# Kernel optimization log

Hardware: AMD Instinct MI355X
Metric: run time of the kernel (lower is better)

## Reference

```python
import jax, jax.numpy as jnp
import numpy as np

B, L, D = 4, 8192, 512


def setup_inputs() -> dict:
    key = jax.random.key(0)
    kx, kwg, kwc = jax.random.split(key, 3)
    x = jax.random.normal(kx, (B, L, D), dtype=jnp.float32)
    # Xavier-uniform init for DxD linears
    bound = float(np.sqrt(6.0 / (D + D)))
    Wg = jax.random.uniform(kwg, (D, D), minval=-bound, maxval=bound, dtype=jnp.float32)
    bg = jnp.ones((D,), dtype=jnp.float32)   # gate bias init to 1.0
    Wc = jax.random.uniform(kwc, (D, D), minval=-bound, maxval=bound, dtype=jnp.float32)
    bc = jnp.zeros((D,), dtype=jnp.float32)
    return {"x": x, "Wg": Wg, "bg": bg, "Wc": Wc, "bc": bc}


def _mingru_scan(gates, cands):
    # h_t = (1 - g_t) * h_{t-1} + g_t * c_t, h_0 = 0
    # linear recurrence h_t = a_t h_{t-1} + b_t with a = 1-g, b = g*c
    a = 1.0 - gates
    b = gates * cands

    def combine(left, right):
        a_l, b_l = left
        a_r, b_r = right
        return a_r * a_l, a_r * b_l + b_r

    _, h = jax.lax.associative_scan(combine, (a, b), axis=1)
    return h


def reference(x, Wg, bg, Wc, bc):
    gates = jax.nn.sigmoid(jnp.einsum('bld,ed->ble', x, Wg) + bg)
    cands = jnp.tanh(jnp.einsum('bld,ed->ble', x, Wc) + bc)
    return _mingru_scan(gates, cands)
```

## Files before the change

kernel.cpp:

```cpp
#include <hip/hip_runtime.h>
#include <stdint.h>
#include <stddef.h>

#define B_ 4
#define L_ 8192
#define D_ 512
#define M_ (B_*L_)
#define K_ 512
#define CHUNK 64
#define NC (L_/CHUNK)

typedef _Float16 f16;
typedef f16 f16x2 __attribute__((ext_vector_type(2)));
typedef f16 f16x4 __attribute__((ext_vector_type(4)));
typedef f16 f16x8 __attribute__((ext_vector_type(8)));
typedef __fp16 h16x2 __attribute__((ext_vector_type(2)));
typedef float f32x4 __attribute__((ext_vector_type(4)));

__device__ __forceinline__ uint32_t pack2(float a, float b) {
  h16x2 p = __builtin_amdgcn_cvt_pkrtz(a, b);
  return __builtin_bit_cast(uint32_t, p);
}

__device__ __forceinline__ void async16(const void* g, void* l) {
  __builtin_amdgcn_global_load_lds(
      (const __attribute__((address_space(1))) uint32_t*)g,
      (__attribute__((address_space(3))) uint32_t*)l,
      16, 0, 0);
}

__global__ __launch_bounds__(256) void cvt_x(const float* __restrict__ x,
                                             f16* __restrict__ xh) {
  int idx = (blockIdx.x * 256 + threadIdx.x) * 4;
  float4 v = *(const float4*)(x + idx);
  f16x4 o = {(f16)v.x, (f16)v.y, (f16)v.z, (f16)v.w};
  *(f16x4*)(xh + idx) = o;
}

__global__ __launch_bounds__(256) void pack_w(const float* __restrict__ Wg,
                                              const float* __restrict__ Wc,
                                              f16* __restrict__ wp) {
  int idx = (blockIdx.x * 256 + threadIdx.x) * 4;
  const float* src = (idx < 262144) ? (Wg + idx) : (Wc + (idx - 262144));
  float4 v = *(const float4*)src;
  f16x4 o = {(f16)v.x, (f16)v.y, (f16)v.z, (f16)v.w};
  *(f16x4*)(wp + idx) = o;
}

__global__ __launch_bounds__(256, 2) void gemm_act(
    const f16* __restrict__ Xh, const f16* __restrict__ Wp,
    const float* __restrict__ bg, const float* __restrict__ bc,
    uint32_t* __restrict__ AC) {
  __shared__ __align__(16) f16 sA[128 * 32];
  __shared__ __align__(16) f16 sBg[128 * 32];
  __shared__ __align__(16) f16 sBc[128 * 32];

  const int tid = threadIdx.x;
  const int id = blockIdx.x;
  const int xcd = id & 7;
  const int slot = id >> 3;
  const int g_ = xcd * 128 + slot;
  const int bm = g_ >> 2;
  const int bn = g_ & 3;

  const int lane = tid & 63;
  const int w = tid >> 6;
  const int wm = w >> 1, wn = w & 1;
  const int l15 = lane & 15, quad = lane >> 4;

  const int srow = tid >> 2;
  const int spc8 = (tid & 3) * 8;
  const f16* gA  = Xh + (size_t)(bm * 128 + srow) * K_ + spc8;
  const f16* gBg = Wp + (size_t)(bn * 128 + srow) * K_ + spc8;
  const f16* gBc = Wp + (size_t)(512 + bn * 128 + srow) * K_ + spc8;
  f16* lA  = sA  + tid * 8;
  f16* lBg = sBg + tid * 8;
  f16* lBc = sBc + tid * 8;

  f32x4 accG[4][4] = {};
  f32x4 accC[4][4] = {};

  for (int k0 = 0; k0 < K_; k0 += 32) {
    async16(gA + k0,  lA);
    async16(gA + (size_t)64 * K_ + k0,  lA  + 64 * 32);
    async16(gBg + k0, lBg);
    async16(gBg + (size_t)64 * K_ + k0, lBg + 64 * 32);
    async16(gBc + k0, lBc);
    async16(gBc + (size_t)64 * K_ + k0, lBc + 64 * 32);
    __syncthreads();

    f16x8 af[4], bgf[4], bcf[4];
#pragma unroll
    for (int i = 0; i < 4; i++)
      af[i]  = *(const f16x8*)(sA  + (wm * 64 + i * 16 + l15) * 32 + quad * 8);
#pragma unroll
    for (int j = 0; j < 4; j++) {
      bgf[j] = *(const f16x8*)(sBg + (wn * 64 + j * 16 + l15) * 32 + quad * 8);
      bcf[j] = *(const f16x8*)(sBc + (wn * 64 + j * 16 + l15) * 32 + quad * 8);
    }
#pragma unroll
    for (int i = 0; i < 4; i++)
#pragma unroll
      for (int j = 0; j < 4; j++) {
        accG[i][j] = __builtin_amdgcn_mfma_f32_16x16x32_f16(af[i], bgf[j], accG[i][j], 0, 0, 0);
        accC[i][j] = __builtin_amdgcn_mfma_f32_16x16x32_f16(af[i], bcf[j], accC[i][j], 0, 0, 0);
      }
    __syncthreads();
  }

#pragma unroll
  for (int j = 0; j < 4; j++) {
    const int col = bn * 128 + wn * 64 + j * 16 + l15;
    const float bgv = bg[col];
    const float bcv = bc[col];
#pragma unroll
    for (int i = 0; i < 4; i++) {
      const int mrow = bm * 128 + wm * 64 + i * 16 + quad * 4;
#pragma unroll
      for (int r = 0; r < 4; r++) {
        float yg = accG[i][j][r] + bgv;
        float yc = accC[i][j][r] + bcv;
        AC[(size_t)(mrow + r) * 512 + col] = pack2(yg, yc);
      }
    }
  }
}

__global__ __launch_bounds__(512) void scan_local(
    uint32_t* __restrict__ AC,
    float* __restrict__ cA, float* __restrict__ cB) {
  const int blk = blockIdx.x;
  const int d = threadIdx.x;
  const size_t base = (size_t)blk * CHUNK * 512 + d;
  float P = 1.0f, Q = 0.0f;
#pragma unroll 4
  for (int t = 0; t < CHUNK; t++) {
    const size_t i = base + (size_t)t * 512;
    f16x2 v = __builtin_bit_cast(f16x2, AC[i]);
    float yg = (float)v[0];
    float yc = (float)v[1];
    float a = 1.0f / (1.0f + __expf(yg));
    float e = __expf(fmaxf(-2.0f * yc, -30.0f));
    float c = (1.0f - e) / (1.0f + e);
    float b = (1.0f - a) * c;
    AC[i] = pack2(a, b);
    Q = fmaf(a, Q, b);
    P *= a;
  }
  cA[blk * 512 + d] = P;
  cB[blk * 512 + d] = Q;
}

__global__ __launch_bounds__(64) void scan_chunks(
    const float* __restrict__ cA, const float* __restrict__ cB,
    float* __restrict__ Hp) {
  const int b = blockIdx.x >> 3;
  const int d = ((blockIdx.x & 7) << 6) + threadIdx.x;
  float h = 0.0f;
#pragma unroll 8
  for (int ch = 0; ch < NC; ch++) {
    const int idx = (b * NC + ch) * 512 + d;
    Hp[idx] = h;
    h = fmaf(cA[idx], h, cB[idx]);
  }
}

__global__ __launch_bounds__(512) void scan_apply(
    const uint32_t* __restrict__ AC, const float* __restrict__ Hp,
    float* __restrict__ out) {
  const int blk = blockIdx.x;
  const int d = threadIdx.x;
  const size_t base = (size_t)blk * CHUNK * 512 + d;
  float h = Hp[blk * 512 + d];
#pragma unroll 4
  for (int t = 0; t < CHUNK; t++) {
    const size_t i = base + (size_t)t * 512;
    f16x2 v = __builtin_bit_cast(f16x2, AC[i]);
    h = fmaf((float)v[0], h, (float)v[1]);
    out[i] = h;
  }
}

extern "C" void kernel_launch(void* const* d_in, const int* in_sizes, int n_in,
                              void* d_out, int out_size, void* d_ws, size_t ws_size,
                              hipStream_t stream) {
  const float* x  = (const float*)d_in[0];
  const float* Wg = (const float*)d_in[1];
  const float* bg = (const float*)d_in[2];
  const float* Wc = (const float*)d_in[3];
  const float* bc = (const float*)d_in[4];
  float* out = (float*)d_out;

  char* ws = (char*)d_ws;
  f16*      xh = (f16*)(ws);
  f16*      wp = (f16*)(ws + 33554432);
  uint32_t* AC = (uint32_t*)(ws + 34603008);
  float*    cA = (float*)(ws + 101711872);
  float*    cB = (float*)(ws + 102760448);
  float*    Hp = (float*)(ws + 103809024);

  cvt_x<<<M_ * D_ / (256 * 4), 256, 0, stream>>>(x, xh);
  pack_w<<<2 * D_ * D_ / (256 * 4), 256, 0, stream>>>(Wg, Wc, wp);
  gemm_act<<<(M_ / 128) * 4, 256, 0, stream>>>(xh, wp, bg, bc, AC);
  scan_local<<<B_ * NC, 512, 0, stream>>>(AC, cA, cB);
  scan_chunks<<<32, 64, 0, stream>>>(cA, cB, Hp);
  scan_apply<<<B_ * NC, 512, 0, stream>>>(AC, Hp, out);
}
```

Measured before the change: 220.9 us.

## Merge prep kernels, parallelize chunk scan with warp shuffles, recompute activations

Merges the x and weight fp16 conversion kernels into one launch. Replaces the serial per-batch chunk-carry scan (32 blocks of 64 threads walking 128 chunks) with a warp-level shuffle scan, one wavefront per (batch, channel). scan_local no longer writes the activated a/b back to AC; scan_apply recomputes the sigmoid/tanh from the raw pre-activations, trading extra transcendental math for fewer global writes. The GEMM launch bound also goes from 2 to 4 blocks per CU, which may force register spilling given its large accumulator arrays.

```diff
diff --git a/kernel.cpp b/kernel.cpp
--- a/kernel.cpp
+++ b/kernel.cpp
@@ -8,7 +8,7 @@
 #define M_ (B_*L_)
 #define K_ 512
 #define CHUNK 64
-#define NC (L_/CHUNK)
+#define NC_SEQ (L_/CHUNK)
 
 typedef _Float16 f16;
 typedef f16 f16x2 __attribute__((ext_vector_type(2)));
@@ -22,6 +22,16 @@
   return __builtin_bit_cast(uint32_t, p);
 }
 
+__device__ __forceinline__ void act_ab(uint32_t raw, float& a, float& b) {
+  f16x2 v = __builtin_bit_cast(f16x2, raw);
+  float yg = (float)v[0];
+  float yc = (float)v[1];
+  a = 1.0f / (1.0f + __expf(yg));
+  float e = __expf(fmaxf(-2.0f * yc, -30.0f));
+  float c = (1.0f - e) / (1.0f + e);
+  b = (1.0f - a) * c;
+}
+
 __device__ __forceinline__ void async16(const void* g, void* l) {
   __builtin_amdgcn_global_load_lds(
       (const __attribute__((address_space(1))) uint32_t*)g,
@@ -29,25 +39,27 @@
       16, 0, 0);
 }
 
-__global__ __launch_bounds__(256) void cvt_x(const float* __restrict__ x,
-                                             f16* __restrict__ xh) {
-  int idx = (blockIdx.x * 256 + threadIdx.x) * 4;
-  float4 v = *(const float4*)(x + idx);
-  f16x4 o = {(f16)v.x, (f16)v.y, (f16)v.z, (f16)v.w};
-  *(f16x4*)(xh + idx) = o;
-}
-
-__global__ __launch_bounds__(256) void pack_w(const float* __restrict__ Wg,
-                                              const float* __restrict__ Wc,
-                                              f16* __restrict__ wp) {
-  int idx = (blockIdx.x * 256 + threadIdx.x) * 4;
-  const float* src = (idx < 262144) ? (Wg + idx) : (Wc + (idx - 262144));
-  float4 v = *(const float4*)src;
-  f16x4 o = {(f16)v.x, (f16)v.y, (f16)v.z, (f16)v.w};
-  *(f16x4*)(wp + idx) = o;
-}
-
-__global__ __launch_bounds__(256, 2) void gemm_act(
+__global__ __launch_bounds__(256) void prep(
+    const float* __restrict__ x, const float* __restrict__ Wg,
+    const float* __restrict__ Wc, f16* __restrict__ xh,
+    f16* __restrict__ wp) {
+  const int blk = blockIdx.x;
+  const int tid = threadIdx.x;
+  if (blk < 16384) {
+    int idx = (blk * 256 + tid) * 4;
+    float4 v = *(const float4*)(x + idx);
+    f16x4 o = {(f16)v.x, (f16)v.y, (f16)v.z, (f16)v.w};
+    *(f16x4*)(xh + idx) = o;
+  } else {
+    int idx = ((blk - 16384) * 256 + tid) * 4;
+    const float* src = (idx < 262144) ? (Wg + idx) : (Wc + (idx - 262144));
+    float4 v = *(const float4*)src;
+    f16x4 o = {(f16)v.x, (f16)v.y, (f16)v.z, (f16)v.w};
+    *(f16x4*)(wp + idx) = o;
+  }
+}
+
+__global__ __launch_bounds__(256, 4) void gemm_act(
     const f16* __restrict__ Xh, const f16* __restrict__ Wp,
     const float* __restrict__ bg, const float* __restrict__ bc,
     uint32_t* __restrict__ AC) {
@@ -127,7 +139,7 @@
 }
 
 __global__ __launch_bounds__(512) void scan_local(
-    uint32_t* __restrict__ AC,
+    const uint32_t* __restrict__ AC,
     float* __restrict__ cA, float* __restrict__ cB) {
   const int blk = blockIdx.x;
   const int d = threadIdx.x;
@@ -135,15 +147,8 @@
   float P = 1.0f, Q = 0.0f;
 #pragma unroll 4
   for (int t = 0; t < CHUNK; t++) {
-    const size_t i = base + (size_t)t * 512;
-    f16x2 v = __builtin_bit_cast(f16x2, AC[i]);
-    float yg = (float)v[0];
-    float yc = (float)v[1];
-    float a = 1.0f / (1.0f + __expf(yg));
-    float e = __expf(fmaxf(-2.0f * yc, -30.0f));
-    float c = (1.0f - e) / (1.0f + e);
-    float b = (1.0f - a) * c;
-    AC[i] = pack2(a, b);
+    float a, b;
+    act_ab(AC[base + (size_t)t * 512], a, b);
     Q = fmaf(a, Q, b);
     P *= a;
   }
@@ -151,18 +156,32 @@
   cB[blk * 512 + d] = Q;
 }
 
-__global__ __launch_bounds__(64) void scan_chunks(
+__global__ __launch_bounds__(256) void scan_mid(
     const float* __restrict__ cA, const float* __restrict__ cB,
     float* __restrict__ Hp) {
-  const int b = blockIdx.x >> 3;
-  const int d = ((blockIdx.x & 7) << 6) + threadIdx.x;
-  float h = 0.0f;
-#pragma unroll 8
-  for (int ch = 0; ch < NC; ch++) {
-    const int idx = (b * NC + ch) * 512 + d;
-    Hp[idx] = h;
-    h = fmaf(cA[idx], h, cB[idx]);
-  }
+  const int wid = blockIdx.x * 4 + (threadIdx.x >> 6);
+  const int lane = threadIdx.x & 63;
+  const int b = wid >> 9;
+  const int d = wid & 511;
+  const int ch0 = lane * 2;
+  const int i0 = (b * NC_SEQ + ch0) * 512 + d;
+  const float Pa = cA[i0],        Qa = cB[i0];
+  const float Pb = cA[i0 + 512],  Qb = cB[i0 + 512];
+  float P = Pa * Pb;
+  float Q = fmaf(Pb, Qa, Qb);
+#pragma unroll
+  for (int off = 1; off < 64; off <<= 1) {
+    float Pp = __shfl_up(P, off, 64);
+    float Qp = __shfl_up(Q, off, 64);
+    if (lane >= off) {
+      Q = fmaf(P, Qp, Q);
+      P = P * Pp;
+    }
+  }
+  float Qe = __shfl_up(Q, 1, 64);
+  if (lane == 0) Qe = 0.0f;
+  Hp[i0] = Qe;
+  Hp[i0 + 512] = fmaf(Pa, Qe, Qa);
 }
 
 __global__ __launch_bounds__(512) void scan_apply(
@@ -175,8 +194,9 @@
 #pragma unroll 4
   for (int t = 0; t < CHUNK; t++) {
     const size_t i = base + (size_t)t * 512;
-    f16x2 v = __builtin_bit_cast(f16x2, AC[i]);
-    h = fmaf((float)v[0], h, (float)v[1]);
+    float a, b;
+    act_ab(AC[i], a, b);
+    h = fmaf(a, h, b);
     out[i] = h;
   }
 }
@@ -199,10 +219,9 @@
   float*    cB = (float*)(ws + 102760448);
   float*    Hp = (float*)(ws + 103809024);
 
-  cvt_x<<<M_ * D_ / (256 * 4), 256, 0, stream>>>(x, xh);
-  pack_w<<<2 * D_ * D_ / (256 * 4), 256, 0, stream>>>(Wg, Wc, wp);
+  prep<<<16896, 256, 0, stream>>>(x, Wg, Wc, xh, wp);
   gemm_act<<<(M_ / 128) * 4, 256, 0, stream>>>(xh, wp, bg, bc, AC);
-  scan_local<<<B_ * NC, 512, 0, stream>>>(AC, cA, cB);
-  scan_chunks<<<32, 64, 0, stream>>>(cA, cB, Hp);
-  scan_apply<<<B_ * NC, 512, 0, stream>>>(AC, Hp, out);
-}
+  scan_local<<<B_ * NC_SEQ, 512, 0, stream>>>(AC, cA, cB);
+  scan_mid<<<512, 256, 0, stream>>>(cA, cB, Hp);
+  scan_apply<<<B_ * NC_SEQ, 512, 0, stream>>>(AC, Hp, out);
+}
```

Result: slower. 496.6 us (+124.8%).
